# Performance work log

Hardware: AMD Instinct MI355X
Metric: run time of the kernel (lower is better)

The kernel has to match this reference:

```python
import jax, jax.numpy as jnp
import numpy as np

B = 131072
FLOW_SIZE = 16
PASS = 8
TRANS = FLOW_SIZE - PASS  # 8
N_BINS = 128
HIDDEN = 256


def setup_inputs() -> dict:
    key = jax.random.key(0)
    k0, k1, k2 = jax.random.split(key, 3)
    x = jax.random.uniform(k0, (B, FLOW_SIZE + 1), dtype=jnp.float32)
    W1 = jax.random.normal(k1, (PASS, HIDDEN), dtype=jnp.float32) * 0.3
    b1 = jnp.zeros((HIDDEN,), dtype=jnp.float32)
    W2 = jax.random.normal(k2, (HIDDEN, TRANS * N_BINS), dtype=jnp.float32) * 0.05
    b2 = jnp.zeros((TRANS * N_BINS,), dtype=jnp.float32)
    return {"x": x, "W1": W1, "b1": b1, "W2": W2, "b2": b2}


def reference(x, W1, b1, W2, b2):
    xA = x[:, :PASS]                      # [B, P]
    xB = x[:, PASS:FLOW_SIZE]             # [B, T]
    jacobian = x[:, FLOW_SIZE:FLOW_SIZE + 1]  # [B, 1]

    # NN: small MLP, exp output -> positive unnormalized bin widths Q [B, T, n_bins]
    h = jax.nn.relu(xA @ W1 + b1)
    Q = jnp.exp(h @ W2 + b2).reshape(x.shape[0], TRANS, N_BINS)

    Qsum = jnp.cumsum(Q, axis=-1)                     # [B, T, n_bins]
    Qnorms = Qsum[:, :, -1:]                          # [B, T, 1]
    Q = Q / (Qnorms / N_BINS)                         # normalized slopes
    Qsum = Qsum / Qnorms                              # normalized CDF
    Qsum = jnp.pad(Qsum, ((0, 0), (0, 0), (1, 0)))    # left-pad CDF with 0

    alphas = xB * N_BINS
    bins = jnp.floor(alphas)
    alphas = (alphas - bins) / N_BINS                 # fractional offset within bin
    bins = jnp.clip(bins.astype(jnp.int32), 0, N_BINS - 1)

    cdf_int_part = jnp.take_along_axis(Qsum, bins[..., None], axis=-1)[..., 0]  # [B, T]
    cdf_float_part = jnp.take_along_axis(Q, bins[..., None], axis=-1)[..., 0]   # [B, T]

    cdf = cdf_float_part * alphas + cdf_int_part      # [B, T]
    jacobian = jacobian * jnp.prod(cdf_float_part, axis=-1, keepdims=True)  # [B, 1]

    return jnp.concatenate((xA, cdf, jacobian), axis=-1)  # [B, flow_size+1]
```

## Files before the change

kernel.cpp:

```cpp
#include <hip/hip_runtime.h>
#include <math.h>

#define NROWS 131072
#define XC    17
#define ROWSB 64
#define HID   256
#define NB    128
#define NCOL  1024
#define LOG2E 1.44269504088896340736f

typedef __attribute__((ext_vector_type(8))) short bf16x8;
typedef __attribute__((ext_vector_type(4))) float f32x4;

#if __has_builtin(__builtin_amdgcn_exp2f)
#define EXP2F(v) __builtin_amdgcn_exp2f(v)
#else
#define EXP2F(v) exp2f(v)
#endif
#if __has_builtin(__builtin_amdgcn_rcpf)
#define RCPF(v) __builtin_amdgcn_rcpf(v)
#else
#define RCPF(v) (1.f / (v))
#endif

__device__ __forceinline__ unsigned short f2bf(float f) {
    unsigned int u = __float_as_uint(f);
    return (unsigned short)((u + 0x7FFFu + ((u >> 16) & 1u)) >> 16);
}

__device__ __forceinline__ float red16(float v) {
    int x;
    x = __builtin_amdgcn_update_dpp(0, __float_as_int(v), 0xB1, 0xF, 0xF, true);
    v += __int_as_float(x);
    x = __builtin_amdgcn_update_dpp(0, __float_as_int(v), 0x4E, 0xF, 0xF, true);
    v += __int_as_float(x);
    x = __builtin_amdgcn_update_dpp(0, __float_as_int(v), 0x141, 0xF, 0xF, true);
    v += __int_as_float(x);
    x = __builtin_amdgcn_update_dpp(0, __float_as_int(v), 0x140, 0xF, 0xF, true);
    v += __int_as_float(x);
    return v;
}

__global__ void prep_w2(const float* __restrict__ W2, unsigned short* __restrict__ w2t) {
    __shared__ __align__(16) unsigned short tkT[32][80];
    const int tid = threadIdx.x;
    const int k0 = (blockIdx.x & 3) * 64;
    const int c0 = (blockIdx.x >> 2) * 32;
    const int c4 = (tid & 7) * 4;
    const int kk = (tid >> 3) * 2;
    const float4 r0 = *(const float4*)&W2[(size_t)(k0 + kk) * NCOL + c0 + c4];
    const float4 r1 = *(const float4*)&W2[(size_t)(k0 + kk + 1) * NCOL + c0 + c4];
    const float v0[4] = {r0.x, r0.y, r0.z, r0.w};
    const float v1[4] = {r1.x, r1.y, r1.z, r1.w};
    #pragma unroll
    for (int i = 0; i < 4; ++i) {
        const unsigned int p = (unsigned int)f2bf(v0[i] * LOG2E)
                             | ((unsigned int)f2bf(v1[i] * LOG2E) << 16);
        *(unsigned int*)&tkT[c4 + i][kk] = p;
    }
    __syncthreads();
    const int g = tid & 7, c = tid >> 3;
    const uint4 q = *(const uint4*)&tkT[c][g * 8];
    *(uint4*)&w2t[(size_t)(c0 + c) * HID + k0 + ((g ^ (c & 7)) << 3)] = q;
}

__global__ __launch_bounds__(256, 4)
void gplc6(const float* __restrict__ x,
           const float* __restrict__ W1,
           const float* __restrict__ b1,
           const unsigned short* __restrict__ w2t,
           const float* __restrict__ b2,
           float* __restrict__ out)
{
    __shared__ float xs[ROWSB * XC];
    __shared__ __align__(16) union {
        unsigned short hb[ROWSB * HID];
        unsigned short w2[2][NB * 64];
    } u;

    const int tid  = threadIdx.x;
    const int lane = tid & 63;
    const int w    = tid >> 6;
    const int quad = lane >> 4;
    const int l15  = lane & 15;
    const int wr   = w * 16;
    const int ksw  = (lane & 7) << 3;
    const size_t r0 = (size_t)blockIdx.x * ROWSB;

    for (int i = tid; i < ROWSB * XC; i += 256) xs[i] = x[r0 * XC + i];
    const int cp = tid & 127, hlf = tid >> 7;
    float w1r[16];
    #pragma unroll
    for (int i = 0; i < 8; ++i) {
        const float2 t2 = *(const float2*)&W1[i * HID + 2 * cp];
        w1r[2 * i] = t2.x; w1r[2 * i + 1] = t2.y;
    }
    const float2 b1v = *(const float2*)&b1[2 * cp];
    __syncthreads();

    for (int r = 0; r < 32; ++r) {
        const int row = hlf * 32 + r;
        float a0 = b1v.x, a1 = b1v.y;
        #pragma unroll
        for (int i = 0; i < 8; ++i) {
            const float xv = xs[row * XC + i];
            a0 = fmaf(xv, w1r[2 * i], a0);
            a1 = fmaf(xv, w1r[2 * i + 1], a1);
        }
        a0 = fmaxf(a0, 0.f); a1 = fmaxf(a1, 0.f);
        const int eidx = row * HID + (((cp >> 2) ^ (row & 15)) << 3) + ((cp & 3) << 1);
        *(unsigned int*)&u.hb[eidx] = (unsigned int)f2bf(a0) | ((unsigned int)f2bf(a1) << 16);
    }
    __syncthreads();

    bf16x8 afr[8];
    #pragma unroll
    for (int kf = 0; kf < 8; ++kf) {
        const int row = wr + l15;
        afr[kf] = *(const bf16x8*)&u.hb[row * HID + (((kf * 4 + quad) ^ l15) << 3)];
    }
    __syncthreads();

    auto stage = [&](int n) {
        const int t = n >> 2, kc = n & 3, buf = n & 1;
        #pragma unroll
        for (int j = 0; j < 4; ++j) {
            const int ob = (w * 4 + j) * 512;
            const int c  = (ob >> 6) + (lane >> 3);
            const int kl = (lane & 7) << 3;
            const unsigned short* gp = w2t + (size_t)(t * NB + c) * HID + kc * 64 + kl;
            unsigned short* lp = &u.w2[buf][ob];
            __builtin_amdgcn_global_load_lds(
                (const __attribute__((address_space(1))) unsigned int*)gp,
                (__attribute__((address_space(3))) unsigned int*)lp, 16, 0, 0);
        }
    };

    float jf[4] = {1.f, 1.f, 1.f, 1.f};

    stage(0);
    #pragma unroll 1
    for (int t = 0; t < 8; ++t) {
        f32x4 acc[8];
        #pragma unroll
        for (int ct = 0; ct < 8; ++ct) acc[ct] = (f32x4){0.f, 0.f, 0.f, 0.f};

        #pragma unroll
        for (int kc = 0; kc < 4; ++kc) {
            __syncthreads();
            const int n = t * 4 + kc;
            if (n < 31) stage(n + 1);
            const unsigned short* wsb = u.w2[kc & 1];
            #pragma unroll
            for (int ks = 0; ks < 2; ++ks) {
                const int kf = kc * 2 + ks;
                const int klog = ks * 32 + quad * 8;
                #pragma unroll
                for (int ct = 0; ct < 8; ++ct) {
                    const int c = ct * 16 + l15;
                    const bf16x8 bf = *(const bf16x8*)&wsb[c * 64 + (klog ^ ksw)];
                    acc[ct] = __builtin_amdgcn_mfma_f32_16x16x32_bf16(afr[kf], bf, acc[ct], 0, 0, 0);
                }
            }
        }

        #pragma unroll
        for (int ct = 0; ct < 8; ++ct) {
            const float bbv = b2[t * NB + ct * 16 + l15] * LOG2E;
            acc[ct][0] += bbv; acc[ct][1] += bbv; acc[ct][2] += bbv; acc[ct][3] += bbv;
        }

        #pragma unroll
        for (int i = 0; i < 4; ++i) {
            const int row = wr + quad * 4 + i;
            const float alpha = xs[row * XC + 8 + t] * 128.f;
            const float fb = floorf(alpha);
            const int bin = min(max((int)fb, 0), 127);
            const float fr = alpha - fb;
            float e[8];
            #pragma unroll
            for (int ct = 0; ct < 8; ++ct) e[ct] = EXP2F(acc[ct][i]);
            const float P1 = e[0],      P2 = P1 + e[1], P3 = P2 + e[2], P4 = P3 + e[3];
            const float P5 = P4 + e[4], P6 = P5 + e[5], P7 = P6 + e[6], P8 = P7 + e[7];
            int thr = (bin - l15 + 15) >> 4;
            thr = min(max(thr, 0), 8);
            const float sA = (thr & 1) ? P1 : 0.f;
            const float sB = (thr & 1) ? P3 : P2;
            const float sC = (thr & 1) ? P5 : P4;
            const float sD = (thr & 1) ? P7 : P6;
            const float sE = (thr & 2) ? sB : sA;
            const float sF = (thr & 2) ? sD : sC;
            float num = (thr & 4) ? sF : sE;
            num = (thr >= 8) ? P8 : num;
            const int cb = bin >> 4;
            const float t1 = (cb & 1) ? e[1] : e[0];
            const float t2 = (cb & 1) ? e[3] : e[2];
            const float t3 = (cb & 1) ? e[5] : e[4];
            const float t4 = (cb & 1) ? e[7] : e[6];
            const float u1 = (cb & 2) ? t2 : t1;
            const float u2 = (cb & 2) ? t4 : t3;
            const float es = (cb & 4) ? u2 : u1;
            float eb  = ((bin & 15) == l15) ? es : 0.f;
            float tot = P8;
            tot = red16(tot); num = red16(num); eb = red16(eb);
            const float inv = RCPF(tot);
            jf[i] *= 128.f * eb * inv;
            if (l15 == 0) xs[row * XC + 8 + t] = fmaf(eb, fr, num) * inv;
        }
    }

    if (l15 == 0) {
        #pragma unroll
        for (int i = 0; i < 4; ++i) {
            const int row = wr + quad * 4 + i;
            xs[row * XC + 16] *= jf[i];
        }
    }
    __syncthreads();
    for (int i = tid; i < ROWSB * XC; i += 256) out[r0 * XC + i] = xs[i];
}

extern "C" void kernel_launch(void* const* d_in, const int* in_sizes, int n_in,
                              void* d_out, int out_size, void* d_ws, size_t ws_size,
                              hipStream_t stream) {
    (void)in_sizes; (void)n_in; (void)ws_size; (void)out_size;
    prep_w2<<<128, 256, 0, stream>>>((const float*)d_in[3], (unsigned short*)d_ws);
    gplc6<<<NROWS / ROWSB, 256, 0, stream>>>(
        (const float*)d_in[0], (const float*)d_in[1], (const float*)d_in[2],
        (const unsigned short*)d_ws, (const float*)d_in[4], (float*)d_out);
}
```

Measured before the change: 164.0 us.

## Halve LDS footprint by chunking hidden activations and W2 staging tiles

Builds the hidden-layer bf16 activations in two 32-row chunks and stages W2 in 64-column by 64-k tiles instead of 128-column tiles, so the shared union drops from 32KB to 16KB. The aim is to fit more resident workgroups per CU and so hide memory latency better. In exchange there are twice as many staging steps and barriers per output tile, plus extra barriers during the hidden-layer build.

```diff
diff --git a/kernel.cpp b/kernel.cpp
--- a/kernel.cpp
+++ b/kernel.cpp
@@ -74,8 +74,8 @@
 {
     __shared__ float xs[ROWSB * XC];
     __shared__ __align__(16) union {
-        unsigned short hb[ROWSB * HID];
-        unsigned short w2[2][NB * 64];
+        unsigned short hb[32 * HID];
+        unsigned short w2[2][64 * 64];
     } u;
 
     const int tid  = threadIdx.x;
@@ -98,38 +98,43 @@
     const float2 b1v = *(const float2*)&b1[2 * cp];
     __syncthreads();
 
-    for (int r = 0; r < 32; ++r) {
-        const int row = hlf * 32 + r;
-        float a0 = b1v.x, a1 = b1v.y;
-        #pragma unroll
-        for (int i = 0; i < 8; ++i) {
-            const float xv = xs[row * XC + i];
-            a0 = fmaf(xv, w1r[2 * i], a0);
-            a1 = fmaf(xv, w1r[2 * i + 1], a1);
-        }
-        a0 = fmaxf(a0, 0.f); a1 = fmaxf(a1, 0.f);
-        const int eidx = row * HID + (((cp >> 2) ^ (row & 15)) << 3) + ((cp & 3) << 1);
-        *(unsigned int*)&u.hb[eidx] = (unsigned int)f2bf(a0) | ((unsigned int)f2bf(a1) << 16);
-    }
-    __syncthreads();
-
     bf16x8 afr[8];
     #pragma unroll
-    for (int kf = 0; kf < 8; ++kf) {
-        const int row = wr + l15;
-        afr[kf] = *(const bf16x8*)&u.hb[row * HID + (((kf * 4 + quad) ^ l15) << 3)];
-    }
-    __syncthreads();
-
-    auto stage = [&](int n) {
-        const int t = n >> 2, kc = n & 3, buf = n & 1;
-        #pragma unroll
-        for (int j = 0; j < 4; ++j) {
-            const int ob = (w * 4 + j) * 512;
-            const int c  = (ob >> 6) + (lane >> 3);
-            const int kl = (lane & 7) << 3;
-            const unsigned short* gp = w2t + (size_t)(t * NB + c) * HID + kc * 64 + kl;
-            unsigned short* lp = &u.w2[buf][ob];
+    for (int ch = 0; ch < 2; ++ch) {
+        for (int r = 0; r < 16; ++r) {
+            const int lrow = hlf * 16 + r;
+            const int row  = ch * 32 + lrow;
+            float a0 = b1v.x, a1 = b1v.y;
+            #pragma unroll
+            for (int i = 0; i < 8; ++i) {
+                const float xv = xs[row * XC + i];
+                a0 = fmaf(xv, w1r[2 * i], a0);
+                a1 = fmaf(xv, w1r[2 * i + 1], a1);
+            }
+            a0 = fmaxf(a0, 0.f); a1 = fmaxf(a1, 0.f);
+            const int eidx = lrow * HID + (((cp >> 2) ^ (row & 15)) << 3) + ((cp & 3) << 1);
+            *(unsigned int*)&u.hb[eidx] = (unsigned int)f2bf(a0) | ((unsigned int)f2bf(a1) << 16);
+        }
+        __syncthreads();
+        if ((w >> 1) == ch) {
+            #pragma unroll
+            for (int kf = 0; kf < 8; ++kf) {
+                const int row = wr + l15;
+                afr[kf] = *(const bf16x8*)&u.hb[(row & 31) * HID + (((kf * 4 + quad) ^ l15) << 3)];
+            }
+        }
+        __syncthreads();
+    }
+
+    auto stage = [&](int m) {
+        const int t = m >> 3, cj = (m >> 2) & 1, kc = m & 3, buf = m & 1;
+        #pragma unroll
+        for (int j = 0; j < 2; ++j) {
+            const int ci  = (w * 2 + j) * 8 + (lane >> 3);
+            const int col = t * NB + cj * 64 + ci;
+            const int kl  = (lane & 7) << 3;
+            const unsigned short* gp = w2t + (size_t)col * HID + kc * 64 + kl;
+            unsigned short* lp = &u.w2[buf][(w * 2 + j) * 512];
             __builtin_amdgcn_global_load_lds(
                 (const __attribute__((address_space(1))) unsigned int*)gp,
                 (__attribute__((address_space(3))) unsigned int*)lp, 16, 0, 0);
@@ -146,20 +151,24 @@
         for (int ct = 0; ct < 8; ++ct) acc[ct] = (f32x4){0.f, 0.f, 0.f, 0.f};
 
         #pragma unroll
-        for (int kc = 0; kc < 4; ++kc) {
-            __syncthreads();
-            const int n = t * 4 + kc;
-            if (n < 31) stage(n + 1);
-            const unsigned short* wsb = u.w2[kc & 1];
-            #pragma unroll
-            for (int ks = 0; ks < 2; ++ks) {
-                const int kf = kc * 2 + ks;
-                const int klog = ks * 32 + quad * 8;
+        for (int cj = 0; cj < 2; ++cj) {
+            #pragma unroll
+            for (int kc = 0; kc < 4; ++kc) {
+                __syncthreads();
+                const int m = t * 8 + cj * 4 + kc;
+                if (m < 63) stage(m + 1);
+                const unsigned short* wsb = u.w2[m & 1];
                 #pragma unroll
-                for (int ct = 0; ct < 8; ++ct) {
-                    const int c = ct * 16 + l15;
-                    const bf16x8 bf = *(const bf16x8*)&wsb[c * 64 + (klog ^ ksw)];
-                    acc[ct] = __builtin_amdgcn_mfma_f32_16x16x32_bf16(afr[kf], bf, acc[ct], 0, 0, 0);
+                for (int ks = 0; ks < 2; ++ks) {
+                    const int kf = kc * 2 + ks;
+                    const int klog = ks * 32 + quad * 8;
+                    #pragma unroll
+                    for (int ci = 0; ci < 4; ++ci) {
+                        const int ct = cj * 4 + ci;
+                        const int c  = ci * 16 + l15;
+                        const bf16x8 bf = *(const bf16x8*)&wsb[c * 64 + (klog ^ ksw)];
+                        acc[ct] = __builtin_amdgcn_mfma_f32_16x16x32_bf16(afr[kf], bf, acc[ct], 0, 0, 0);
+                    }
                 }
             }
         }
```

Result: slower. 169.5 us (+3.4%).
